# Performance work log

Hardware: AMD Instinct MI355X
Metric: run time of the kernel (lower is better)

## Reference

```python
import jax, jax.numpy as jnp
import numpy as np

LATENT_DIM = 256
BOOK_SIZE = 8192


def setup_inputs() -> dict:
    key = jax.random.key(0)
    k1, k2 = jax.random.split(key)
    z_e = jax.random.normal(k1, (16, LATENT_DIM, 32, 32), dtype=jnp.float32)
    codebook = jax.random.normal(k2, (BOOK_SIZE, LATENT_DIM), dtype=jnp.float32)
    return {"z_e": z_e, "codebook": codebook}


def reference(z_e, codebook):
    # NCHW -> NHWC -> (B*H*W, D)
    flat_z = jnp.transpose(z_e, (0, 2, 3, 1)).reshape(-1, LATENT_DIM)
    # squared euclidean distance via matmul: ||z||^2 + ||e||^2 - 2 z.e
    dist = (
        jnp.sum(flat_z ** 2, axis=1, keepdims=True)
        + jnp.sum(codebook ** 2, axis=1)
        - 2.0 * flat_z @ codebook.T
    )  # (N, book_size)
    indices = jnp.argmin(dist, axis=1)          # (N,)
    z_q = codebook[indices]                      # (N, D) gather
    return z_q, indices
```

## Files before the change

### kernel.cpp

```cpp
#include <hip/hip_runtime.h>
#include <stdint.h>

#define NROWS 16384
#define NCODES 8192
#define DIM 256
#define EPS_S 0.4f
#define SM 0.5f

typedef __attribute__((ext_vector_type(8))) short bf16x8;
typedef __attribute__((ext_vector_type(16))) float f32x16;
typedef unsigned int uint32;

__device__ __forceinline__ unsigned short f2bf(float f) {
  union { float f; unsigned int u; } v; v.f = f;
  unsigned int u = v.u;
  return (unsigned short)((u + 0x7FFFu + ((u >> 16) & 1u)) >> 16);
}

__device__ __forceinline__ unsigned long long packdi(float d, int idx) {
  unsigned int u = __float_as_uint(d);
  u = (u & 0x80000000u) ? ~u : (u | 0x80000000u);
  return ((unsigned long long)u << 32) | (unsigned int)idx;
}
__device__ __forceinline__ unsigned long long u64min(unsigned long long a,
                                                     unsigned long long b) {
  return a < b ? a : b;
}
__device__ __forceinline__ unsigned long long shflx64(unsigned long long v, int m) {
  int lo = __shfl_xor((int)(unsigned int)v, m);
  int hi = __shfl_xor((int)(v >> 32), m);
  return ((unsigned long long)(unsigned int)hi << 32) | (unsigned int)lo;
}
__device__ __forceinline__ uint32 umax(uint32 a, uint32 b) { return a > b ? a : b; }
__device__ __forceinline__ uint32 umin(uint32 a, uint32 b) { return a < b ? a : b; }

__device__ __forceinline__ void glds16(const ushort* g, ushort* l) {
  __builtin_amdgcn_global_load_lds(
      (const __attribute__((address_space(1))) unsigned int*)g,
      (__attribute__((address_space(3))) unsigned int*)l, 16, 0, 0);
}

__global__ __launch_bounds__(256) void prep(const float* __restrict__ z,
                                            const float* __restrict__ cb,
                                            float* __restrict__ flatz,
                                            ushort* __restrict__ zb,
                                            ushort* __restrict__ eb,
                                            float* __restrict__ enorm) {
  __shared__ float t[32][33];
  const int blk = blockIdx.x;
  if (blk < 4096) {
    const int tx = threadIdx.x & 31, ty = threadIdx.x >> 5;
    const int ht = blk & 31, ct = (blk >> 5) & 7, b = blk >> 8;
    const float* src = z + (size_t)b * 262144 + (size_t)(ct * 32) * 1024 + ht * 32;
#pragma unroll
    for (int i = 0; i < 4; ++i) {
      int c = ty + i * 8;
      t[c][tx] = src[c * 1024 + tx];
    }
    __syncthreads();
    const int r = threadIdx.x >> 3, q = threadIdx.x & 7;
    float4 vv;
    vv.x = t[q * 4 + 0][r];
    vv.y = t[q * 4 + 1][r];
    vv.z = t[q * 4 + 2][r];
    vv.w = t[q * 4 + 3][r];
    const int row = b * 1024 + ht * 32 + r;
    *(float4*)(flatz + (size_t)row * 256 + ct * 32 + q * 4) = vv;
    ushort4 o;
    o.x = f2bf(vv.x); o.y = f2bf(vv.y); o.z = f2bf(vv.z); o.w = f2bf(vv.w);
    *(ushort4*)(zb + (size_t)row * 256 + ct * 32 + q * 4) = o;
  } else {
    const int lane = threadIdx.x & 63, wave = threadIdx.x >> 6;
    const int code = (blk - 4096) * 4 + wave;
    float4 v = *(const float4*)(cb + (size_t)code * 256 + lane * 4);
    ushort4 o;
    o.x = f2bf(v.x); o.y = f2bf(v.y); o.z = f2bf(v.z); o.w = f2bf(v.w);
    *(ushort4*)(eb + (size_t)code * 256 + lane * 4) = o;
    float ss = v.x * v.x + v.y * v.y + v.z * v.z + v.w * v.w;
#pragma unroll
    for (int s = 1; s < 64; s <<= 1) ss += __shfl_xor(ss, s);
    if (lane == 0) enorm[code] = ss;
  }
}

__device__ __forceinline__ void init_acc(f32x16 acc[4][2],
                                         const float* __restrict__ epb,
                                         int wm, int lg) {
#pragma unroll
  for (int m = 0; m < 4; ++m) {
    const float* ep = epb + wm * 128 + m * 32 + 4 * lg;
    float4 e0 = *(const float4*)(ep);
    float4 e1 = *(const float4*)(ep + 8);
    float4 e2 = *(const float4*)(ep + 16);
    float4 e3 = *(const float4*)(ep + 24);
    f32x16 c0;
    c0[0]  = 1024.f - 0.5f * e0.x; c0[1]  = 1024.f - 0.5f * e0.y;
    c0[2]  = 1024.f - 0.5f * e0.z; c0[3]  = 1024.f - 0.5f * e0.w;
    c0[4]  = 1024.f - 0.5f * e1.x; c0[5]  = 1024.f - 0.5f * e1.y;
    c0[6]  = 1024.f - 0.5f * e1.z; c0[7]  = 1024.f - 0.5f * e1.w;
    c0[8]  = 1024.f - 0.5f * e2.x; c0[9]  = 1024.f - 0.5f * e2.y;
    c0[10] = 1024.f - 0.5f * e2.z; c0[11] = 1024.f - 0.5f * e2.w;
    c0[12] = 1024.f - 0.5f * e3.x; c0[13] = 1024.f - 0.5f * e3.y;
    c0[14] = 1024.f - 0.5f * e3.z; c0[15] = 1024.f - 0.5f * e3.w;
    acc[m][0] = c0; acc[m][1] = c0;
  }
}

__device__ __forceinline__ void epilogue(const f32x16 acc[4][2],
                                         uint32* __restrict__ bm, int cid0b,
                                         int zrowb, int wm, int wn,
                                         int l31, int lg) {
  const int cid0 = cid0b + wm * 8;
#pragma unroll
  for (int n = 0; n < 2; ++n) {
    uint32 res[8];
#pragma unroll
    for (int m = 0; m < 4; ++m)
#pragma unroll
      for (int hc = 0; hc < 2; ++hc) {
        uint32 m1 = 0, m2 = 0;
#pragma unroll
        for (int p = 0; p < 8; ++p) {
          uint32 id = (uint32)((p & 3) | (lg << 2) | ((p >> 2) << 3));
          uint32 pv = (__float_as_uint(acc[m][n][hc * 8 + p]) & ~31u) | id;
          m2 = umax(m2, umin(m1, pv));
          m1 = umax(m1, pv);
        }
        uint32 o1 = (uint32)__shfl_xor((int)m1, 32);
        uint32 o2 = (uint32)__shfl_xor((int)m2, 32);
        m2 = umax(umax(m2, o2), umin(m1, o1));
        m1 = umax(m1, o1);
        float s1 = __uint_as_float(m1 & ~31u);
        float s2 = __uint_as_float(m2 & ~31u);
        res[m * 2 + hc] = (s1 - s2 > SM) ? (m1 | 16u) : m1;
      }
    const int zr = zrowb + wn * 64 + n * 32 + l31;
    uint4 o;
    o.x = lg ? res[4] : res[0];
    o.y = lg ? res[5] : res[1];
    o.z = lg ? res[6] : res[2];
    o.w = lg ? res[7] : res[3];
    *(uint4*)(bm + (size_t)zr * 512 + cid0 + lg * 4) = o;
  }
}

__global__ __launch_bounds__(512, 2) void vq_gemm(const ushort* __restrict__ eb,
                                                  const ushort* __restrict__ zb,
                                                  const float* __restrict__ enorm,
                                                  uint32* __restrict__ bm) {
  __shared__ __align__(16) ushort Am[65536];
  __shared__ __align__(16) ushort Bsr[16384];
  const int tid = threadIdx.x;
  const int wave = tid >> 6, lane = tid & 63;
  const int wm = wave >> 2, wn = wave & 3;
  const int l31 = lane & 31, lg = lane >> 5;
  const int cg = blockIdx.x & 31, yg = blockIdx.x >> 5;
  const int code0 = cg * 256;
  const int zrow00 = yg * 2048;
  const int cid0b = cg * 16;

#pragma unroll
  for (int j = 0; j < 16; ++j) {
    const int u = tid + j * 512;
    const int row = u >> 5;
    const int g = (u & 31) ^ (row & 7);
    glds16(eb + (size_t)(code0 + row) * 256 + g * 8,
           Am + (wave * 64 + j * 512) * 8);
  }

  const int u0 = tid, u1 = tid + 512;
  const ushort* bU0 = zb + (size_t)(zrow00 + (u0 >> 2)) * 256 +
                      ((u0 & 3) ^ ((u0 >> 3) & 3)) * 8;
  const ushort* bU1 = zb + (size_t)(zrow00 + (u1 >> 2)) * 256 +
                      ((u1 & 3) ^ ((u1 >> 3) & 3)) * 8;
  ushort* bL = Bsr + wave * 512;

  glds16(bU0, bL);
  glds16(bU1, bL + 4096);

  asm volatile("s_waitcnt vmcnt(0)" ::: "memory");
  __syncthreads();

  f32x16 acc[4][2];
  init_acc(acc, enorm + code0, wm, lg);

  const int swzA = l31 & 7;
  const int arow = (wm * 128 + l31) * 256;
  const int swzB = (l31 >> 1) & 3;
  const int colu0 = ((0 | lg) ^ swzB) * 8;
  const int colu1 = ((2 | lg) ^ swzB) * 8;
  const int brow_u = (wn * 64 + l31) * 32;

#pragma unroll 1
  for (int yp = 0; yp < 8; ++yp) {
    if (yp > 0) {
      epilogue(acc, bm, cid0b, zrow00 + (yp - 1) * 256, wm, wn, l31, lg);
      init_acc(acc, enorm + code0, wm, lg);
    }
#pragma unroll
    for (int kc = 0; kc < 8; ++kc) {
      const int c = yp * 8 + kc;
      const int slot = c & 1;
      if (c < 63) {
        const int cn = c + 1;
        const size_t off = (size_t)(cn >> 3) * 65536 + (size_t)(cn & 7) * 32;
        glds16(bU0 + off, bL + (slot ^ 1) * 8192);
        glds16(bU1 + off, bL + (slot ^ 1) * 8192 + 4096);
      }
      bf16x8 a0[4], a1[4], b0[2], b1[2];
#pragma unroll
      for (int m = 0; m < 4; ++m) {
        a0[m] = *(const bf16x8*)&Am[arow + m * 8192 +
                                    (((kc * 4 + 0) | lg) ^ swzA) * 8];
        a1[m] = *(const bf16x8*)&Am[arow + m * 8192 +
                                    (((kc * 4 + 2) | lg) ^ swzA) * 8];
      }
#pragma unroll
      for (int n = 0; n < 2; ++n) {
        b0[n] = *(const bf16x8*)&Bsr[slot * 8192 + brow_u + n * 1024 + colu0];
        b1[n] = *(const bf16x8*)&Bsr[slot * 8192 + brow_u + n * 1024 + colu1];
      }
      __builtin_amdgcn_s_setprio(1);
#pragma unroll
      for (int m = 0; m < 4; ++m)
#pragma unroll
        for (int n = 0; n < 2; ++n)
          acc[m][n] = __builtin_amdgcn_mfma_f32_32x32x16_bf16(a0[m], b0[n],
                                                              acc[m][n], 0, 0, 0);
#pragma unroll
      for (int m = 0; m < 4; ++m)
#pragma unroll
        for (int n = 0; n < 2; ++n)
          acc[m][n] = __builtin_amdgcn_mfma_f32_32x32x16_bf16(a1[m], b1[n],
                                                              acc[m][n], 0, 0, 0);
      __builtin_amdgcn_s_setprio(0);
      if (c < 63) {
        asm volatile("s_waitcnt vmcnt(0)" ::: "memory");
        __builtin_amdgcn_s_barrier();
        asm volatile("" ::: "memory");
      }
    }
  }
  epilogue(acc, bm, cid0b, zrow00 + 7 * 256, wm, wn, l31, lg);
}

__device__ __forceinline__ unsigned long long chunk_exact(
    int chunk, const float* __restrict__ zrow, const float* __restrict__ cb,
    const float* __restrict__ enorm, int lane) {
  const int code = chunk * 16 + (lane >> 2);
  const float* zp = zrow + (lane & 3) * 64;
  const float* cp = cb + (size_t)code * 256 + (lane & 3) * 64;
  float s = 0.f;
#pragma unroll
  for (int d = 0; d < 64; d += 4) {
    float4 zv = *(const float4*)(zp + d);
    float4 cv = *(const float4*)(cp + d);
    s = fmaf(zv.x, cv.x, s); s = fmaf(zv.y, cv.y, s);
    s = fmaf(zv.z, cv.z, s); s = fmaf(zv.w, cv.w, s);
  }
  s += __shfl_xor(s, 1);
  s += __shfl_xor(s, 2);
  float dist = fmaf(-2.f, s, enorm[code]);
  unsigned long long key = ((lane & 3) == 0) ? packdi(dist, code) : ~0ull;
#pragma unroll
  for (int m = 1; m < 64; m <<= 1) key = u64min(key, shflx64(key, m));
  return key;
}

__global__ __launch_bounds__(256) void vq_sel(const uint32* __restrict__ bm,
                                              const float* __restrict__ flatz,
                                              const float* __restrict__ cb,
                                              const float* __restrict__ enorm,
                                              float* __restrict__ zq,
                                              float* __restrict__ oidx) {
  const int lane = threadIdx.x & 63;
  const int row = blockIdx.x * 4 + (threadIdx.x >> 6);
  uint4 va = *(const uint4*)(bm + (size_t)row * 512 + lane * 8);
  uint4 vb = *(const uint4*)(bm + (size_t)row * 512 + lane * 8 + 4);
  uint32 v[8] = {va.x, va.y, va.z, va.w, vb.x, vb.y, vb.z, vb.w};
  uint32 m1 = 0, m2 = 0; int ch = 0;
#pragma unroll
  for (int s = 0; s < 8; ++s) {
    uint32 pv = v[s];
    m2 = umax(m2, umin(m1, pv));
    ch = (pv > m1) ? (lane * 8 + s) : ch;
    m1 = umax(m1, pv);
  }
#pragma unroll
  for (int m = 1; m < 64; m <<= 1) {
    uint32 o1 = (uint32)__shfl_xor((int)m1, m);
    uint32 o2 = (uint32)__shfl_xor((int)m2, m);
    int oc = __shfl_xor(ch, m);
    m2 = umax(umax(m2, o2), umin(m1, o1));
    ch = (o1 > m1) ? oc : ch;
    m1 = umax(m1, o1);
  }
  float s1 = __uint_as_float(m1 & ~31u);
  float s2 = __uint_as_float(m2 & ~31u);
  int idx;
  if ((m1 & 16u) && (s1 - s2 > SM)) {
    idx = ch * 16 + (int)(m1 & 15u);
  } else {
    const float* zrow = flatz + (size_t)row * 256;
    unsigned long long key = chunk_exact(ch, zrow, cb, enorm, lane);
    float dbest;
    { unsigned int u = (unsigned int)(key >> 32);
      u = (u & 0x80000000u) ? (u & 0x7FFFFFFFu) : ~u;
      dbest = __uint_as_float(u); }
    float thr = (1024.f - 0.5f * dbest) - EPS_S;
#pragma unroll
    for (int s = 0; s < 8; ++s) {
      bool cand = __uint_as_float(v[s] & ~31u) >= thr;
      unsigned long long mk = __ballot(cand);
      while (mk) {
        int L = __ffsll(mk) - 1;
        mk &= mk - 1;
        int c2 = L * 8 + s;
        if (c2 == ch) continue;
        key = u64min(key, chunk_exact(c2, zrow, cb, enorm, lane));
      }
    }
    idx = (int)(key & 0xFFFFFFFFull);
  }
  if (lane == 0) oidx[row] = (float)idx;
  float4 val = *(const float4*)(cb + (size_t)idx * 256 + lane * 4);
  *(float4*)(zq + (size_t)row * 256 + lane * 4) = val;
}

extern "C" void kernel_launch(void* const* d_in, const int* in_sizes, int n_in,
                              void* d_out, int out_size, void* d_ws, size_t ws_size,
                              hipStream_t stream) {
  const float* z = (const float*)d_in[0];
  const float* cb = (const float*)d_in[1];
  char* ws = (char*)d_ws;
  ushort* zb = (ushort*)(ws);
  ushort* eb = (ushort*)(ws + (8u << 20));
  float* enorm = (float*)(ws + (12u << 20));
  uint32* bm = (uint32*)(ws + (13u << 20));
  float* zq = (float*)d_out;
  float* oidx = zq + (size_t)NROWS * DIM;
  float* flatz = zq;

  prep<<<4096 + NCODES / 4, 256, 0, stream>>>(z, cb, flatz, zb, eb, enorm);
  vq_gemm<<<256, 512, 0, stream>>>(eb, zb, enorm, bm);
  vq_sel<<<NROWS / 4, 256, 0, stream>>>(bm, flatz, cb, enorm, zq, oidx);
}
```

Before: 177.3 us.

## Give each wave private z rows and drop per-step block barriers in VQ GEMM

Changes the wave tiling from a 2x4 grid (128 codes x 64 rows per wave) to each wave owning 32 z rows across all 256 codes. Each wave now loads its own B slice into a private LDS region, so the per-k-step s_barrier is removed and only a vmcnt wait stays. The cost is more A-fragment LDS reads per wave (8 A tiles against 1 B tile), which raises LDS bandwidth pressure and register use for A operands.

```diff
diff --git a/kernel.cpp b/kernel.cpp
--- a/kernel.cpp
+++ b/kernel.cpp
@@ -83,12 +83,12 @@
   }
 }
 
-__device__ __forceinline__ void init_acc(f32x16 acc[4][2],
+__device__ __forceinline__ void init_acc(f32x16 acc[8],
                                          const float* __restrict__ epb,
-                                         int wm, int lg) {
-#pragma unroll
-  for (int m = 0; m < 4; ++m) {
-    const float* ep = epb + wm * 128 + m * 32 + 4 * lg;
+                                         int lg) {
+#pragma unroll
+  for (int m = 0; m < 8; ++m) {
+    const float* ep = epb + m * 32 + 4 * lg;
     float4 e0 = *(const float4*)(ep);
     float4 e1 = *(const float4*)(ep + 8);
     float4 e2 = *(const float4*)(ep + 16);
@@ -102,46 +102,47 @@
     c0[10] = 1024.f - 0.5f * e2.z; c0[11] = 1024.f - 0.5f * e2.w;
     c0[12] = 1024.f - 0.5f * e3.x; c0[13] = 1024.f - 0.5f * e3.y;
     c0[14] = 1024.f - 0.5f * e3.z; c0[15] = 1024.f - 0.5f * e3.w;
-    acc[m][0] = c0; acc[m][1] = c0;
-  }
-}
-
-__device__ __forceinline__ void epilogue(const f32x16 acc[4][2],
+    acc[m] = c0;
+  }
+}
+
+__device__ __forceinline__ void epilogue(const f32x16 acc[8],
                                          uint32* __restrict__ bm, int cid0b,
-                                         int zrowb, int wm, int wn,
-                                         int l31, int lg) {
-  const int cid0 = cid0b + wm * 8;
-#pragma unroll
-  for (int n = 0; n < 2; ++n) {
-    uint32 res[8];
-#pragma unroll
-    for (int m = 0; m < 4; ++m)
-#pragma unroll
-      for (int hc = 0; hc < 2; ++hc) {
-        uint32 m1 = 0, m2 = 0;
-#pragma unroll
-        for (int p = 0; p < 8; ++p) {
-          uint32 id = (uint32)((p & 3) | (lg << 2) | ((p >> 2) << 3));
-          uint32 pv = (__float_as_uint(acc[m][n][hc * 8 + p]) & ~31u) | id;
-          m2 = umax(m2, umin(m1, pv));
-          m1 = umax(m1, pv);
-        }
-        uint32 o1 = (uint32)__shfl_xor((int)m1, 32);
-        uint32 o2 = (uint32)__shfl_xor((int)m2, 32);
-        m2 = umax(umax(m2, o2), umin(m1, o1));
-        m1 = umax(m1, o1);
-        float s1 = __uint_as_float(m1 & ~31u);
-        float s2 = __uint_as_float(m2 & ~31u);
-        res[m * 2 + hc] = (s1 - s2 > SM) ? (m1 | 16u) : m1;
-      }
-    const int zr = zrowb + wn * 64 + n * 32 + l31;
-    uint4 o;
-    o.x = lg ? res[4] : res[0];
-    o.y = lg ? res[5] : res[1];
-    o.z = lg ? res[6] : res[2];
-    o.w = lg ? res[7] : res[3];
-    *(uint4*)(bm + (size_t)zr * 512 + cid0 + lg * 4) = o;
-  }
+                                         int zrowb, int wave, int l31, int lg) {
+  uint32 res[16];
+#pragma unroll
+  for (int m = 0; m < 8; ++m)
+#pragma unroll
+    for (int hc = 0; hc < 2; ++hc) {
+      uint32 m1 = 0, m2 = 0;
+#pragma unroll
+      for (int p = 0; p < 8; ++p) {
+        uint32 id = (uint32)((p & 3) | (lg << 2) | ((p >> 2) << 3));
+        uint32 pv = (__float_as_uint(acc[m][hc * 8 + p]) & ~31u) | id;
+        m2 = umax(m2, umin(m1, pv));
+        m1 = umax(m1, pv);
+      }
+      uint32 o1 = (uint32)__shfl_xor((int)m1, 32);
+      uint32 o2 = (uint32)__shfl_xor((int)m2, 32);
+      m2 = umax(umax(m2, o2), umin(m1, o1));
+      m1 = umax(m1, o1);
+      float s1 = __uint_as_float(m1 & ~31u);
+      float s2 = __uint_as_float(m2 & ~31u);
+      res[m * 2 + hc] = (s1 - s2 > SM) ? (m1 | 16u) : m1;
+    }
+  const int zr = zrowb + wave * 32 + l31;
+  uint32* dst = bm + (size_t)zr * 512 + cid0b + lg * 8;
+  uint4 oA, oB;
+  oA.x = lg ? res[8]  : res[0];
+  oA.y = lg ? res[9]  : res[1];
+  oA.z = lg ? res[10] : res[2];
+  oA.w = lg ? res[11] : res[3];
+  oB.x = lg ? res[12] : res[4];
+  oB.y = lg ? res[13] : res[5];
+  oB.z = lg ? res[14] : res[6];
+  oB.w = lg ? res[15] : res[7];
+  *(uint4*)(dst) = oA;
+  *(uint4*)(dst + 4) = oB;
 }
 
 __global__ __launch_bounds__(512, 2) void vq_gemm(const ushort* __restrict__ eb,
@@ -149,10 +150,9 @@
                                                   const float* __restrict__ enorm,
                                                   uint32* __restrict__ bm) {
   __shared__ __align__(16) ushort Am[65536];
-  __shared__ __align__(16) ushort Bsr[16384];
+  __shared__ __align__(16) ushort Bp[16384];
   const int tid = threadIdx.x;
   const int wave = tid >> 6, lane = tid & 63;
-  const int wm = wave >> 2, wn = wave & 3;
   const int l31 = lane & 31, lg = lane >> 5;
   const int cg = blockIdx.x & 31, yg = blockIdx.x >> 5;
   const int code0 = cg * 256;
@@ -168,80 +168,68 @@
            Am + (wave * 64 + j * 512) * 8);
   }
 
-  const int u0 = tid, u1 = tid + 512;
-  const ushort* bU0 = zb + (size_t)(zrow00 + (u0 >> 2)) * 256 +
-                      ((u0 & 3) ^ ((u0 >> 3) & 3)) * 8;
-  const ushort* bU1 = zb + (size_t)(zrow00 + (u1 >> 2)) * 256 +
-                      ((u1 & 3) ^ ((u1 >> 3) & 3)) * 8;
-  ushort* bL = Bsr + wave * 512;
-
-  glds16(bU0, bL);
-  glds16(bU1, bL + 4096);
+  const ushort* bS0 = zb + (size_t)(zrow00 + wave * 32 + (lane >> 2)) * 256 +
+                      (((lane & 3) ^ ((lane >> 3) & 3))) * 8;
+  const ushort* bS1 = bS0 + 16 * 256;
+  ushort* Bw = Bp + wave * 2048;
+
+  glds16(bS0, Bw);
+  glds16(bS1, Bw + 512);
 
   asm volatile("s_waitcnt vmcnt(0)" ::: "memory");
   __syncthreads();
 
-  f32x16 acc[4][2];
-  init_acc(acc, enorm + code0, wm, lg);
+  f32x16 acc[8];
+  init_acc(acc, enorm + code0, lg);
 
   const int swzA = l31 & 7;
-  const int arow = (wm * 128 + l31) * 256;
   const int swzB = (l31 >> 1) & 3;
   const int colu0 = ((0 | lg) ^ swzB) * 8;
   const int colu1 = ((2 | lg) ^ swzB) * 8;
-  const int brow_u = (wn * 64 + l31) * 32;
+  const int browp = l31 * 32;
 
 #pragma unroll 1
   for (int yp = 0; yp < 8; ++yp) {
     if (yp > 0) {
-      epilogue(acc, bm, cid0b, zrow00 + (yp - 1) * 256, wm, wn, l31, lg);
-      init_acc(acc, enorm + code0, wm, lg);
+      epilogue(acc, bm, cid0b, zrow00 + (yp - 1) * 256, wave, l31, lg);
+      init_acc(acc, enorm + code0, lg);
     }
 #pragma unroll
     for (int kc = 0; kc < 8; ++kc) {
       const int c = yp * 8 + kc;
-      const int slot = c & 1;
+      const int s = c & 1;
       if (c < 63) {
-        const int cn = c + 1;
-        const size_t off = (size_t)(cn >> 3) * 65536 + (size_t)(cn & 7) * 32;
-        glds16(bU0 + off, bL + (slot ^ 1) * 8192);
-        glds16(bU1 + off, bL + (slot ^ 1) * 8192 + 4096);
-      }
-      bf16x8 a0[4], a1[4], b0[2], b1[2];
-#pragma unroll
-      for (int m = 0; m < 4; ++m) {
-        a0[m] = *(const bf16x8*)&Am[arow + m * 8192 +
+        const size_t off = (size_t)((c + 1) >> 3) * 65536 +
+                           (size_t)((c + 1) & 7) * 32;
+        glds16(bS0 + off, Bw + (s ^ 1) * 1024);
+        glds16(bS1 + off, Bw + (s ^ 1) * 1024 + 512);
+      }
+      bf16x8 a0[8], a1[8], b0, b1;
+#pragma unroll
+      for (int m = 0; m < 8; ++m) {
+        a0[m] = *(const bf16x8*)&Am[(m * 32 + l31) * 256 +
                                     (((kc * 4 + 0) | lg) ^ swzA) * 8];
-        a1[m] = *(const bf16x8*)&Am[arow + m * 8192 +
+        a1[m] = *(const bf16x8*)&Am[(m * 32 + l31) * 256 +
                                     (((kc * 4 + 2) | lg) ^ swzA) * 8];
       }
-#pragma unroll
-      for (int n = 0; n < 2; ++n) {
-        b0[n] = *(const bf16x8*)&Bsr[slot * 8192 + brow_u + n * 1024 + colu0];
-        b1[n] = *(const bf16x8*)&Bsr[slot * 8192 + brow_u + n * 1024 + colu1];
-      }
+      b0 = *(const bf16x8*)&Bp[wave * 2048 + s * 1024 + browp + colu0];
+      b1 = *(const bf16x8*)&Bp[wave * 2048 + s * 1024 + browp + colu1];
       __builtin_amdgcn_s_setprio(1);
 #pragma unroll
-      for (int m = 0; m < 4; ++m)
-#pragma unroll
-        for (int n = 0; n < 2; ++n)
-          acc[m][n] = __builtin_amdgcn_mfma_f32_32x32x16_bf16(a0[m], b0[n],
-                                                              acc[m][n], 0, 0, 0);
-#pragma unroll
-      for (int m = 0; m < 4; ++m)
-#pragma unroll
-        for (int n = 0; n < 2; ++n)
-          acc[m][n] = __builtin_amdgcn_mfma_f32_32x32x16_bf16(a1[m], b1[n],
-                                                              acc[m][n], 0, 0, 0);
+      for (int m = 0; m < 8; ++m)
+        acc[m] = __builtin_amdgcn_mfma_f32_32x32x16_bf16(a0[m], b0, acc[m],
+                                                         0, 0, 0);
+#pragma unroll
+      for (int m = 0; m < 8; ++m)
+        acc[m] = __builtin_amdgcn_mfma_f32_32x32x16_bf16(a1[m], b1, acc[m],
+                                                         0, 0, 0);
       __builtin_amdgcn_s_setprio(0);
       if (c < 63) {
         asm volatile("s_waitcnt vmcnt(0)" ::: "memory");
-        __builtin_amdgcn_s_barrier();
-        asm volatile("" ::: "memory");
-      }
-    }
-  }
-  epilogue(acc, bm, cid0b, zrow00 + 7 * 256, wm, wn, l31, lg);
+      }
+    }
+  }
+  epilogue(acc, bm, cid0b, zrow00 + 7 * 256, wave, l31, lg);
 }
 
 __device__ __forceinline__ unsigned long long chunk_exact(
```

Measured after the change: 200.4 us. 13.0% more time.
